# Kernel optimization log

Hardware: AMD Instinct MI355X
Metric: run time of the kernel (lower is better)

## Reference

```python
import jax, jax.numpy as jnp
import numpy as np

B, S, D, U = 32, 2048, 1024, 1024


def setup_inputs() -> dict:
    key = jax.random.key(0)
    ks = jax.random.split(key, 7)
    scale = 1.0 / np.sqrt(D)
    return {
        "query": jax.random.normal(ks[0], (B, D), dtype=jnp.float32),
        "values": jax.random.normal(ks[1], (B, S, D), dtype=jnp.float32),
        "w1": jax.random.normal(ks[2], (D, U), dtype=jnp.float32) * scale,
        "b1": jnp.zeros((U,), dtype=jnp.float32),
        "w2": jax.random.normal(ks[3], (D, U), dtype=jnp.float32) * scale,
        "b2": jnp.zeros((U,), dtype=jnp.float32),
        "wv": jax.random.normal(ks[4], (U, 1), dtype=jnp.float32) * (1.0 / np.sqrt(U)),
        "bv": jnp.zeros((1,), dtype=jnp.float32),
    }


def reference(query, values, w1, b1, w2, b2, wv, bv):
    # q_proj: [B, 1, U]; v_proj: [B, S, U]
    q_proj = (query @ w1 + b1)[:, None, :]
    v_proj = jnp.einsum("bsd,du->bsu", values, w2) + b2
    # score: [B, S, 1]
    score = jnp.tanh(q_proj + v_proj) @ wv + bv
    attention_weights = jax.nn.softmax(score, axis=1)  # softmax over seq axis
    context_vector = jnp.sum(attention_weights * values, axis=1)  # [B, D]
    return (context_vector, attention_weights)
```

## Files before the change

kernel.cpp:

```cpp
#include <hip/hip_runtime.h>
#include <hip/hip_bf16.h>

#define BB 32
#define SS 2048
#define DD 1024
#define UU 1024
#define MBLK 64

typedef short bf16x8 __attribute__((ext_vector_type(8)));
typedef float f32x4 __attribute__((ext_vector_type(4)));
typedef int i32x4 __attribute__((ext_vector_type(4)));
typedef unsigned short u16x4 __attribute__((ext_vector_type(4)));
typedef unsigned int u32;
typedef unsigned short u16;

__device__ __forceinline__ unsigned short f2bf(float x) {
    union { float f; unsigned int u; } v; v.f = x;
    unsigned int r = v.u + 0x7fffu + ((v.u >> 16) & 1u);
    return (unsigned short)(r >> 16);
}

__device__ __forceinline__ f32x4 ntload4(const float* p) {
    return __builtin_nontemporal_load(reinterpret_cast<const f32x4*>(p));
}

__device__ __forceinline__ u32 cvtpk(float lo, float hi) {
    u32 r;
    asm("v_cvt_pk_bf16_f32 %0, %1, %2" : "=v"(r) : "v"(lo), "v"(hi));
    return r;
}

__device__ __forceinline__ float bf2f(u16 h) {
    union { unsigned int u; float f; } v; v.u = ((unsigned int)h) << 16;
    return v.f;
}

__global__ void zero_kernel(float* __restrict__ qp2) {
    qp2[blockIdx.x * 256 + threadIdx.x] = 0.f;
}

__global__ void qproj_kernel(const float* __restrict__ query, const float* __restrict__ w1,
                             const float* __restrict__ b1, const float* __restrict__ b2,
                             float* __restrict__ qp2) {
    __shared__ float qs[4][128];
    const int uc = blockIdx.x;
    const int bg = blockIdx.y;
    const int ds = blockIdx.z;
    const int t = threadIdx.x;
    if (t < 128) {
#pragma unroll
        for (int bi = 0; bi < 4; ++bi)
            qs[bi][t] = query[(bg * 4 + bi) * DD + ds * 128 + t];
    }
    __syncthreads();
    const int u = uc * 256 + t;
    float a0 = 0.f, a1 = 0.f, a2 = 0.f, a3 = 0.f;
    const float* wp = w1 + (size_t)(ds * 128) * UU + u;
#pragma unroll 4
    for (int d = 0; d < 128; ++d) {
        const float w = wp[(size_t)d * UU];
        a0 = fmaf(qs[0][d], w, a0);
        a1 = fmaf(qs[1][d], w, a1);
        a2 = fmaf(qs[2][d], w, a2);
        a3 = fmaf(qs[3][d], w, a3);
    }
    const float bb = (ds == 0) ? (b1[u] + b2[u]) : 0.f;
    atomicAdd(&qp2[(bg * 4 + 0) * UU + u], a0 + bb);
    atomicAdd(&qp2[(bg * 4 + 1) * UU + u], a1 + bb);
    atomicAdd(&qp2[(bg * 4 + 2) * UU + u], a2 + bb);
    atomicAdd(&qp2[(bg * 4 + 3) * UU + u], a3 + bb);
}

__global__ void w2q_kernel(const float* __restrict__ w2, unsigned short* __restrict__ w2q) {
    __shared__ float tile[64][65];
    const int k0 = (blockIdx.x >> 4) * 64;
    const int u0 = (blockIdx.x & 15) * 64;
    const int t = threadIdx.x;
    {
        const int kr = t >> 2, uc = (t & 3) * 16;
        const float* src = w2 + (size_t)(k0 + kr) * UU + u0 + uc;
#pragma unroll
        for (int j = 0; j < 4; ++j) {
            f32x4 v = *reinterpret_cast<const f32x4*>(src + j * 4);
            tile[kr][uc + j * 4 + 0] = v[0]; tile[kr][uc + j * 4 + 1] = v[1];
            tile[kr][uc + j * 4 + 2] = v[2]; tile[kr][uc + j * 4 + 3] = v[3];
        }
    }
    __syncthreads();
    const int c = t >> 5;
    const int uqL = c >> 1, ksL = c & 1;
    const int uq = (u0 >> 4) + uqL, ks = (k0 >> 5) + ksL;
#pragma unroll
    for (int li = 0; li < 2; ++li) {
        const int l = (t & 31) * 2 + li;
        const int colL = uqL * 16 + (l & 15);
        const int kL = ksL * 32 + (l >> 4) * 8;
        bf16x8 pk;
#pragma unroll
        for (int e = 0; e < 8; ++e) pk[e] = (short)f2bf(tile[kL + e][colL]);
        *reinterpret_cast<bf16x8*>(&w2q[(size_t)(((uq * 32 + ks) * 64 + l)) * 8]) = pk;
    }
}

__global__ __launch_bounds__(1024, 4)
void score_kernel(const float* __restrict__ values, const unsigned short* __restrict__ w2q,
                  const float* __restrict__ qp2, const float* __restrict__ wv,
                  const float* __restrict__ bv, float* __restrict__ score,
                  unsigned short* __restrict__ vbf) {
    __shared__ __align__(16) unsigned short Apk[MBLK * DD];
    __shared__ float ssum[16][MBLK];

    const int blk = blockIdx.x;
    const int b = blk >> 5;
    const int s0 = (blk & 31) * MBLK;
    const int tid = threadIdx.x;
    const int lane = tid & 63;
    const int wid = tid >> 6;
    const int arow = lane & 15;
    const int uq0 = wid * 4;

    const int row = tid >> 4;
    const int g = tid & 15;
    const int q = g & 3;
    const int lsw = ((row & 15) + 16 * q) ^ q;
    const size_t elem0 = ((size_t)b * SS + s0 + row) * DD + g * 8;
    const float* src = values + elem0;
    unsigned short* vdst = vbf ? (vbf + elem0) : nullptr;
    unsigned short* sdst = Apk + (size_t)(g >> 2) * 2048 + (size_t)(row >> 4) * 512 + lsw * 8;

#define STAGE_W(p, x, y)                                                       \
    {                                                                          \
        u32 q0 = cvtpk((x)[0], (x)[1]), q1 = cvtpk((x)[2], (x)[3]);            \
        u32 q2 = cvtpk((y)[0], (y)[1]), q3 = cvtpk((y)[2], (y)[3]);            \
        i32x4 w_ = {(int)q0, (int)q1, (int)q2, (int)q3};                       \
        *reinterpret_cast<i32x4*>(sdst + (size_t)(p) * 8192) = w_;             \
        if (vdst)                                                              \
            __builtin_nontemporal_store(                                       \
                w_, reinterpret_cast<i32x4*>(vdst + (size_t)(p) * 128));       \
    }

    const unsigned short* Ab = Apk + (size_t)(lane ^ ((lane >> 4) & 3)) * 8;
    const unsigned short* wqs =
        w2q + ((size_t)__builtin_amdgcn_readfirstlane(wid) << 16);
    const size_t lane8 = (size_t)lane * 8;

    f32x4 acc[4][4];
#pragma unroll
    for (int mf = 0; mf < 4; ++mf)
#pragma unroll
        for (int nf = 0; nf < 4; ++nf) { f32x4 z = {0.f, 0.f, 0.f, 0.f}; acc[mf][nf] = z; }

    {
        f32x4 x0 = ntload4(src), y0 = ntload4(src + 4);
        STAGE_W(0, x0, y0);
    }
    __syncthreads();

#pragma unroll 1
    for (int p = 0; p < 8; ++p) {
        f32x4 L0, L1;
        if (p < 7) {
            const float* s1 = src + (p + 1) * 128;
            L0 = ntload4(s1);
            L1 = ntload4(s1 + 4);
        }
#pragma unroll
        for (int kk = 0; kk < 4; ++kk) {
            const int ks = p * 4 + kk;
            bf16x8 aF[4];
#pragma unroll
            for (int mf = 0; mf < 4; ++mf)
                aF[mf] = *reinterpret_cast<const bf16x8*>(Ab + ((size_t)(ks * 4 + mf) << 9));
            bf16x8 bF[4];
#pragma unroll
            for (int nf = 0; nf < 4; ++nf)
                bF[nf] = *reinterpret_cast<const bf16x8*>(
                    wqs + (((size_t)(nf * 32 + ks)) << 9) + lane8);
#pragma unroll
            for (int mf = 0; mf < 4; ++mf)
#pragma unroll
                for (int nf = 0; nf < 4; ++nf)
                    acc[mf][nf] = __builtin_amdgcn_mfma_f32_16x16x32_bf16(
                        aF[mf], bF[nf], acc[mf][nf], 0, 0, 0);
        }
        if (p < 7) {
            STAGE_W(p + 1, L0, L1);
            __syncthreads();
        }
    }
#undef STAGE_W

    float rowsum[16];
#pragma unroll
    for (int i = 0; i < 16; ++i) rowsum[i] = 0.f;
#pragma unroll
    for (int nf = 0; nf < 4; ++nf) {
        const int u = (uq0 + nf) * 16 + arow;
        const float qv = qp2[b * UU + u];
        const float wvv = wv[u];
#pragma unroll
        for (int mf = 0; mf < 4; ++mf)
#pragma unroll
            for (int i = 0; i < 4; ++i) {
                float h = acc[mf][nf][i] + qv;
                float e = __expf(2.f * h);
                float th = 1.f - 2.f / (e + 1.f);
                rowsum[mf * 4 + i] = fmaf(th, wvv, rowsum[mf * 4 + i]);
            }
    }
#pragma unroll
    for (int i = 0; i < 16; ++i) {
        float v = rowsum[i];
        v += __shfl_xor(v, 1);
        v += __shfl_xor(v, 2);
        v += __shfl_xor(v, 4);
        v += __shfl_xor(v, 8);
        rowsum[i] = v;
    }
    if ((lane & 15) == 0) {
        const int rg = lane >> 4;
#pragma unroll
        for (int mf = 0; mf < 4; ++mf)
#pragma unroll
            for (int i = 0; i < 4; ++i)
                ssum[wid][mf * 16 + rg * 4 + i] = rowsum[mf * 4 + i];
    }
    __syncthreads();
    if (tid < MBLK) {
        float sc = bv[0];
#pragma unroll
        for (int w = 0; w < 16; ++w) sc += ssum[w][tid];
        score[b * SS + s0 + tid] = sc;
    }
}

__global__ void softmax_kernel(const float* __restrict__ score, float* __restrict__ weights) {
    __shared__ float red[8];
    const int b = blockIdx.x;
    const int t = threadIdx.x;
    float local[8];
    float mx = -1e30f;
#pragma unroll
    for (int i = 0; i < 8; ++i) {
        local[i] = score[b * SS + i * 256 + t];
        mx = fmaxf(mx, local[i]);
    }
    for (int off = 1; off < 64; off <<= 1) mx = fmaxf(mx, __shfl_xor(mx, off));
    if ((t & 63) == 0) red[t >> 6] = mx;
    __syncthreads();
    const float m = fmaxf(fmaxf(red[0], red[1]), fmaxf(red[2], red[3]));
    float sum = 0.f;
#pragma unroll
    for (int i = 0; i < 8; ++i) {
        local[i] = __expf(local[i] - m);
        sum += local[i];
    }
    for (int off = 1; off < 64; off <<= 1) sum += __shfl_xor(sum, off);
    if ((t & 63) == 0) red[4 + (t >> 6)] = sum;
    __syncthreads();
    const float inv = 1.f / (red[4] + red[5] + red[6] + red[7]);
#pragma unroll
    for (int i = 0; i < 8; ++i) weights[b * SS + i * 256 + t] = local[i] * inv;
}

__global__ void context_kernel(const float* __restrict__ values, const float* __restrict__ weights,
                               float* __restrict__ ctx) {
    __shared__ float ws[SS];
    __shared__ f32x4 red[16][16];
    const int b = blockIdx.x;
    const int dc = blockIdx.y;
    const int t = threadIdx.x;
    for (int i = t; i < SS; i += 256) ws[i] = weights[b * SS + i];
    __syncthreads();
    const int dt = t & 15;
    const int ph = t >> 4;
    const int d = dc * 64 + dt * 4;
    const float* vb = values + (size_t)b * SS * DD + d;
    f32x4 acc = {0.f, 0.f, 0.f, 0.f};
#pragma unroll 8
    for (int s = ph; s < SS; s += 16) {
        const float w = ws[s];
        f32x4 v = ntload4(vb + (size_t)s * DD);
        acc[0] = fmaf(w, v[0], acc[0]);
        acc[1] = fmaf(w, v[1], acc[1]);
        acc[2] = fmaf(w, v[2], acc[2]);
        acc[3] = fmaf(w, v[3], acc[3]);
    }
    red[ph][dt] = acc;
    __syncthreads();
    if (t < 16) {
        f32x4 r = red[0][t];
#pragma unroll
        for (int w = 1; w < 16; ++w) {
            f32x4 x = red[w][t];
#pragma unroll
            for (int i = 0; i < 4; ++i) r[i] += x[i];
        }
        *reinterpret_cast<f32x4*>(ctx + (size_t)b * DD + dc * 64 + t * 4) = r;
    }
}

__global__ void context_bf16_kernel(const unsigned short* __restrict__ vbf,
                                    const float* __restrict__ weights,
                                    float* __restrict__ ctx) {
    __shared__ float ws[SS];
    __shared__ f32x4 red[16][16];
    const int b = blockIdx.x;
    const int dc = blockIdx.y;
    const int t = threadIdx.x;
    for (int i = t; i < SS; i += 256) ws[i] = weights[b * SS + i];
    __syncthreads();
    const int dt = t & 15;
    const int ph = t >> 4;
    const int d = dc * 64 + dt * 4;
    const unsigned short* vb = vbf + (size_t)b * SS * DD + d;
    f32x4 acc = {0.f, 0.f, 0.f, 0.f};
#pragma unroll 8
    for (int s = ph; s < SS; s += 16) {
        const float w = ws[s];
        u16x4 v = __builtin_nontemporal_load(
            reinterpret_cast<const u16x4*>(vb + (size_t)s * DD));
        acc[0] = fmaf(w, bf2f(v[0]), acc[0]);
        acc[1] = fmaf(w, bf2f(v[1]), acc[1]);
        acc[2] = fmaf(w, bf2f(v[2]), acc[2]);
        acc[3] = fmaf(w, bf2f(v[3]), acc[3]);
    }
    red[ph][dt] = acc;
    __syncthreads();
    if (t < 16) {
        f32x4 r = red[0][t];
#pragma unroll
        for (int w = 1; w < 16; ++w) {
            f32x4 x = red[w][t];
#pragma unroll
            for (int i = 0; i < 4; ++i) r[i] += x[i];
        }
        *reinterpret_cast<f32x4*>(ctx + (size_t)b * DD + dc * 64 + t * 4) = r;
    }
}

extern "C" void kernel_launch(void* const* d_in, const int* in_sizes, int n_in,
                              void* d_out, int out_size, void* d_ws, size_t ws_size,
                              hipStream_t stream) {
    const float* query  = (const float*)d_in[0];
    const float* values = (const float*)d_in[1];
    const float* w1     = (const float*)d_in[2];
    const float* b1     = (const float*)d_in[3];
    const float* w2     = (const float*)d_in[4];
    const float* b2     = (const float*)d_in[5];
    const float* wv     = (const float*)d_in[6];
    const float* bv     = (const float*)d_in[7];

    float* ctx     = (float*)d_out;
    float* weights = (float*)d_out + (size_t)BB * DD;

    float* qp2           = (float*)d_ws;
    unsigned short* w2q  = (unsigned short*)((char*)d_ws + 131072);
    float* score         = (float*)((char*)d_ws + 131072 + 2097152);

    const size_t vbf_off = 131072 + 2097152 + 262144;
    const size_t vbf_bytes = (size_t)BB * SS * DD * 2;
    unsigned short* vbf = (ws_size >= vbf_off + vbf_bytes)
                              ? (unsigned short*)((char*)d_ws + vbf_off)
                              : nullptr;

    zero_kernel<<<dim3(BB * UU / 256), 256, 0, stream>>>(qp2);
    qproj_kernel<<<dim3(4, 8, 8), 256, 0, stream>>>(query, w1, b1, b2, qp2);
    w2q_kernel<<<dim3(256), 256, 0, stream>>>(w2, w2q);
    score_kernel<<<dim3(BB * SS / MBLK), 1024, 0, stream>>>(values, w2q, qp2, wv, bv, score, vbf);
    softmax_kernel<<<dim3(BB), 256, 0, stream>>>(score, weights);
    if (vbf)
        context_bf16_kernel<<<dim3(BB, 16), 256, 0, stream>>>(vbf, weights, ctx);
    else
        context_kernel<<<dim3(BB, 16), 256, 0, stream>>>(values, weights, ctx);
}
```

Before: 232.0 us.

## Switch score GEMM from 16x16x32 to 32x32x16 bf16 MFMA with new layouts

Replaces the 4x4 grid of 16x16x32 MFMAs per wave with a 2x2 grid of 32x32x16 MFMAs. The W2 prepack and the LDS layout for values are rearranged to match the new operand fragment shapes, with an XOR swizzle to avoid bank conflicts. The tanh/wv epilogue is remapped to the 32x32 accumulator layout, with one extra shuffle stage. The aim is fewer LDS fragment loads per FLOP and fewer MFMA issues per FLOP. The cost is a more complex row mapping in the epilogue, where an error would give wrong scores.

```diff
diff --git a/kernel.cpp b/kernel.cpp
--- a/kernel.cpp
+++ b/kernel.cpp
@@ -9,6 +9,7 @@
 
 typedef short bf16x8 __attribute__((ext_vector_type(8)));
 typedef float f32x4 __attribute__((ext_vector_type(4)));
+typedef float f32x16 __attribute__((ext_vector_type(16)));
 typedef int i32x4 __attribute__((ext_vector_type(4)));
 typedef unsigned short u16x4 __attribute__((ext_vector_type(4)));
 typedef unsigned int u32;
@@ -71,7 +72,7 @@
     atomicAdd(&qp2[(bg * 4 + 3) * UU + u], a3 + bb);
 }
 
-__global__ void w2q_kernel(const float* __restrict__ w2, unsigned short* __restrict__ w2q) {
+__global__ void w2r_kernel(const float* __restrict__ w2, unsigned short* __restrict__ w2r) {
     __shared__ float tile[64][65];
     const int k0 = (blockIdx.x >> 4) * 64;
     const int u0 = (blockIdx.x & 15) * 64;
@@ -87,23 +88,25 @@
         }
     }
     __syncthreads();
-    const int c = t >> 5;
-    const int uqL = c >> 1, ksL = c & 1;
-    const int uq = (u0 >> 4) + uqL, ks = (k0 >> 5) + ksL;
 #pragma unroll
     for (int li = 0; li < 2; ++li) {
-        const int l = (t & 31) * 2 + li;
-        const int colL = uqL * 16 + (l & 15);
-        const int kL = ksL * 32 + (l >> 4) * 8;
+        const int slot = t * 2 + li;
+        const int ub_l = slot >> 8;
+        const int ks_l = (slot >> 6) & 3;
+        const int l = slot & 63;
+        const int colL = ub_l * 32 + (l & 31);
+        const int kL = ks_l * 16 + (l >> 5) * 8;
         bf16x8 pk;
 #pragma unroll
         for (int e = 0; e < 8; ++e) pk[e] = (short)f2bf(tile[kL + e][colL]);
-        *reinterpret_cast<bf16x8*>(&w2q[(size_t)(((uq * 32 + ks) * 64 + l)) * 8]) = pk;
+        const int ub = (u0 >> 5) + ub_l;
+        const int ks = (k0 >> 4) + ks_l;
+        *reinterpret_cast<bf16x8*>(&w2r[(size_t)((ub * 64 + ks) * 64 + l) * 8]) = pk;
     }
 }
 
 __global__ __launch_bounds__(1024, 4)
-void score_kernel(const float* __restrict__ values, const unsigned short* __restrict__ w2q,
+void score_kernel(const float* __restrict__ values, const unsigned short* __restrict__ w2r,
                   const float* __restrict__ qp2, const float* __restrict__ wv,
                   const float* __restrict__ bv, float* __restrict__ score,
                   unsigned short* __restrict__ vbf) {
@@ -116,17 +119,15 @@
     const int tid = threadIdx.x;
     const int lane = tid & 63;
     const int wid = tid >> 6;
-    const int arow = lane & 15;
-    const int uq0 = wid * 4;
 
     const int row = tid >> 4;
     const int g = tid & 15;
-    const int q = g & 3;
-    const int lsw = ((row & 15) + 16 * q) ^ q;
+    const int hof = g >> 1;
+    const int lw = ((row & 31) + 32 * (g & 1)) ^ hof;
     const size_t elem0 = ((size_t)b * SS + s0 + row) * DD + g * 8;
     const float* src = values + elem0;
     unsigned short* vdst = vbf ? (vbf + elem0) : nullptr;
-    unsigned short* sdst = Apk + (size_t)(g >> 2) * 2048 + (size_t)(row >> 4) * 512 + lsw * 8;
+    unsigned short* sdst = Apk + (size_t)hof * 1024 + (size_t)(row >> 5) * 512 + lw * 8;
 
 #define STAGE_W(p, x, y)                                                       \
     {                                                                          \
@@ -139,16 +140,17 @@
                 w_, reinterpret_cast<i32x4*>(vdst + (size_t)(p) * 128));       \
     }
 
-    const unsigned short* Ab = Apk + (size_t)(lane ^ ((lane >> 4) & 3)) * 8;
     const unsigned short* wqs =
-        w2q + ((size_t)__builtin_amdgcn_readfirstlane(wid) << 16);
+        w2r + ((size_t)__builtin_amdgcn_readfirstlane(wid) << 16);
     const size_t lane8 = (size_t)lane * 8;
 
-    f32x4 acc[4][4];
-#pragma unroll
-    for (int mf = 0; mf < 4; ++mf)
-#pragma unroll
-        for (int nf = 0; nf < 4; ++nf) { f32x4 z = {0.f, 0.f, 0.f, 0.f}; acc[mf][nf] = z; }
+    f32x16 acc[2][2];
+#pragma unroll
+    for (int mg = 0; mg < 2; ++mg)
+#pragma unroll
+        for (int ng = 0; ng < 2; ++ng)
+#pragma unroll
+            for (int r = 0; r < 16; ++r) acc[mg][ng][r] = 0.f;
 
     {
         f32x4 x0 = ntload4(src), y0 = ntload4(src + 4);
@@ -165,23 +167,22 @@
             L1 = ntload4(s1 + 4);
         }
 #pragma unroll
-        for (int kk = 0; kk < 4; ++kk) {
-            const int ks = p * 4 + kk;
-            bf16x8 aF[4];
-#pragma unroll
-            for (int mf = 0; mf < 4; ++mf)
-                aF[mf] = *reinterpret_cast<const bf16x8*>(Ab + ((size_t)(ks * 4 + mf) << 9));
-            bf16x8 bF[4];
-#pragma unroll
-            for (int nf = 0; nf < 4; ++nf)
-                bF[nf] = *reinterpret_cast<const bf16x8*>(
-                    wqs + (((size_t)(nf * 32 + ks)) << 9) + lane8);
-#pragma unroll
-            for (int mf = 0; mf < 4; ++mf)
-#pragma unroll
-                for (int nf = 0; nf < 4; ++nf)
-                    acc[mf][nf] = __builtin_amdgcn_mfma_f32_16x16x32_bf16(
-                        aF[mf], bF[nf], acc[mf][nf], 0, 0, 0);
+        for (int ksl = 0; ksl < 8; ++ksl) {
+            const int ks16 = p * 8 + ksl;
+            bf16x8 aF[2];
+#pragma unroll
+            for (int mg = 0; mg < 2; ++mg)
+                aF[mg] = *reinterpret_cast<const bf16x8*>(
+                    Apk + (size_t)ks16 * 1024 + mg * 512 + (size_t)(lane ^ ksl) * 8);
+            bf16x8 bF[2];
+#pragma unroll
+            for (int ng = 0; ng < 2; ++ng)
+                bF[ng] = *reinterpret_cast<const bf16x8*>(
+                    wqs + (((size_t)(ng * 64 + ks16)) << 9) + lane8);
+            acc[0][0] = __builtin_amdgcn_mfma_f32_32x32x16_bf16(aF[0], bF[0], acc[0][0], 0, 0, 0);
+            acc[0][1] = __builtin_amdgcn_mfma_f32_32x32x16_bf16(aF[0], bF[1], acc[0][1], 0, 0, 0);
+            acc[1][0] = __builtin_amdgcn_mfma_f32_32x32x16_bf16(aF[1], bF[0], acc[1][0], 0, 0, 0);
+            acc[1][1] = __builtin_amdgcn_mfma_f32_32x32x16_bf16(aF[1], bF[1], acc[1][1], 0, 0, 0);
         }
         if (p < 7) {
             STAGE_W(p + 1, L0, L1);
@@ -190,40 +191,43 @@
     }
 #undef STAGE_W
 
-    float rowsum[16];
-#pragma unroll
-    for (int i = 0; i < 16; ++i) rowsum[i] = 0.f;
-#pragma unroll
-    for (int nf = 0; nf < 4; ++nf) {
-        const int u = (uq0 + nf) * 16 + arow;
+    const int hi = lane >> 5;
+    float rowsum[32];
+#pragma unroll
+    for (int i = 0; i < 32; ++i) rowsum[i] = 0.f;
+#pragma unroll
+    for (int ng = 0; ng < 2; ++ng) {
+        const int u = wid * 64 + ng * 32 + (lane & 31);
         const float qv = qp2[b * UU + u];
         const float wvv = wv[u];
 #pragma unroll
-        for (int mf = 0; mf < 4; ++mf)
-#pragma unroll
-            for (int i = 0; i < 4; ++i) {
-                float h = acc[mf][nf][i] + qv;
-                float e = __expf(2.f * h);
+        for (int mg = 0; mg < 2; ++mg)
+#pragma unroll
+            for (int r = 0; r < 16; ++r) {
+                float hv = acc[mg][ng][r] + qv;
+                float e = __expf(2.f * hv);
                 float th = 1.f - 2.f / (e + 1.f);
-                rowsum[mf * 4 + i] = fmaf(th, wvv, rowsum[mf * 4 + i]);
+                rowsum[mg * 16 + r] = fmaf(th, wvv, rowsum[mg * 16 + r]);
             }
     }
 #pragma unroll
-    for (int i = 0; i < 16; ++i) {
+    for (int i = 0; i < 32; ++i) {
         float v = rowsum[i];
         v += __shfl_xor(v, 1);
         v += __shfl_xor(v, 2);
         v += __shfl_xor(v, 4);
         v += __shfl_xor(v, 8);
+        v += __shfl_xor(v, 16);
         rowsum[i] = v;
     }
-    if ((lane & 15) == 0) {
-        const int rg = lane >> 4;
-#pragma unroll
-        for (int mf = 0; mf < 4; ++mf)
-#pragma unroll
-            for (int i = 0; i < 4; ++i)
-                ssum[wid][mf * 16 + rg * 4 + i] = rowsum[mf * 4 + i];
+    if ((lane & 31) == 0) {
+#pragma unroll
+        for (int mg = 0; mg < 2; ++mg)
+#pragma unroll
+            for (int r = 0; r < 16; ++r) {
+                const int rw = mg * 32 + (r & 3) + 8 * (r >> 2) + 4 * hi;
+                ssum[wid][rw] = rowsum[mg * 16 + r];
+            }
     }
     __syncthreads();
     if (tid < MBLK) {
@@ -355,7 +359,7 @@
     float* weights = (float*)d_out + (size_t)BB * DD;
 
     float* qp2           = (float*)d_ws;
-    unsigned short* w2q  = (unsigned short*)((char*)d_ws + 131072);
+    unsigned short* w2r  = (unsigned short*)((char*)d_ws + 131072);
     float* score         = (float*)((char*)d_ws + 131072 + 2097152);
 
     const size_t vbf_off = 131072 + 2097152 + 262144;
@@ -366,8 +370,8 @@
 
     zero_kernel<<<dim3(BB * UU / 256), 256, 0, stream>>>(qp2);
     qproj_kernel<<<dim3(4, 8, 8), 256, 0, stream>>>(query, w1, b1, b2, qp2);
-    w2q_kernel<<<dim3(256), 256, 0, stream>>>(w2, w2q);
-    score_kernel<<<dim3(BB * SS / MBLK), 1024, 0, stream>>>(values, w2q, qp2, wv, bv, score, vbf);
+    w2r_kernel<<<dim3(256), 256, 0, stream>>>(w2, w2r);
+    score_kernel<<<dim3(BB * SS / MBLK), 1024, 0, stream>>>(values, w2r, qp2, wv, bv, score, vbf);
     softmax_kernel<<<dim3(BB), 256, 0, stream>>>(score, weights);
     if (vbf)
         context_bf16_kernel<<<dim3(BB, 16), 256, 0, stream>>>(vbf, weights, ctx);
```

Measured after the change: 250.2 us. 1.08x slower.
